# Kernel optimization log

Measured on AMD Instinct MI355X. Metric: run time of the kernel, lower is better.

The kernel has to match this reference:

```python
import jax, jax.numpy as jnp
import numpy as np

B, S, D, F = 8, 2048, 256, 8

def setup_inputs() -> dict:
    key = jax.random.key(0)
    ks = jax.random.split(key, 7)
    hidden_states = jax.random.normal(ks[0], (B, S, D), dtype=jnp.float32)
    # flat indices into zero-prepended [1 + B*S, D] token table; 0 = padding row
    select_idx = jax.random.randint(ks[1], (B, S, F), 0, B * S + 1, dtype=jnp.int32)
    word_mask = jax.random.randint(ks[2], (B, S), 0, 2, dtype=jnp.int32)
    W1 = jax.random.normal(ks[3], (D, D), dtype=jnp.float32) * (1.0 / np.sqrt(D))
    b1 = jax.random.normal(ks[4], (D,), dtype=jnp.float32) * 0.02
    w2 = jax.random.normal(ks[5], (D,), dtype=jnp.float32) * (1.0 / np.sqrt(D))
    b2 = jax.random.normal(ks[6], (1,), dtype=jnp.float32) * 0.02
    return {"hidden_states": hidden_states, "select_idx": select_idx,
            "word_mask": word_mask, "W1": W1, "b1": b1, "w2": w2, "b2": b2}

def reference(hidden_states, select_idx, word_mask, W1, b1, w2, b2):
    b, s, d = hidden_states.shape
    h = jnp.tanh(hidden_states.reshape(-1, d) @ W1.T + b1)          # [B*S, D]
    h = jnp.concatenate([jnp.zeros((1, d), h.dtype), h], axis=0)    # zero padding row at index 0
    g = h[select_idx.reshape(-1)]                                    # gather: [B*S*F, D]
    g = g.reshape(b * s, -1, d).max(axis=1)                          # AdaptiveMaxPool1d(1) over word occurrences
    scores = (g @ w2 + b2[0]).reshape(b, s)                          # w2 linear -> [B, S]
    neg = -10000.0 * (1.0 - word_mask.astype(jnp.float32))
    return scores.astype(jnp.float32) + neg
```

## Files before the change

kernel.cpp:

```cpp
#include <hip/hip_runtime.h>
#include <hip/hip_bf16.h>
#include <math.h>

#define BB 8
#define SS 2048
#define DD 256
#define FF 8
#define NTOK (BB*SS)

typedef __bf16 bf16x8 __attribute__((ext_vector_type(8)));
typedef float  f32x4  __attribute__((ext_vector_type(4)));
typedef float  f32x2  __attribute__((ext_vector_type(2)));

#define BM 128
#define BN 64
#define BK 64
#define NSTEP (DD/BK)
#define XS 72

__device__ __forceinline__ float fast_tanh(float x) {
    float e = __expf(2.0f * x);
    return 1.0f - 2.0f * __builtin_amdgcn_rcpf(e + 1.0f);
}

__device__ __forceinline__ unsigned pack2_bf16(float a, float b) {
    return (__float_as_uint(a) >> 16) | (__float_as_uint(b) & 0xFFFF0000u);
}

__device__ __forceinline__ unsigned char f32_to_fp8(float v) {
    return (unsigned char)(__builtin_amdgcn_cvt_pk_fp8_f32(v, v, 0, false) & 0xFF);
}

__global__ __launch_bounds__(512, 4) void gemm_tanh_kernel(
    const float* __restrict__ x, const float* __restrict__ W1,
    const float* __restrict__ b1, unsigned char* __restrict__ table)
{
    __shared__ __align__(16) unsigned short xs[2][BM * XS];
    __shared__ __align__(16) unsigned short wsb[2][BN * XS];

    const int tid  = threadIdx.x;
    const int bx   = blockIdx.x;
    const int tokgrp = bx & 127;
    const int nblk   = bx >> 7;
    const int tok0 = tokgrp * BM;
    const int n0   = nblk * BN;

    if (bx == 0 && tid < 64) ((unsigned int*)table)[tid] = 0u;

    const int wave = tid >> 6, lane = tid & 63;
    const int wm = wave >> 1;
    const int wn = wave & 1;
    const int lr = lane & 15;
    const int kg = lane >> 4;

    f32x4 xr[4], wr[2];

    auto load_chunk = [&](int k0) {
        #pragma unroll
        for (int rep = 0; rep < 4; ++rep) {
            int slot = rep * 512 + tid;
            int row = slot >> 4, kc = slot & 15;
            xr[rep] = *(const f32x4*)&x[(size_t)(tok0 + row) * DD + k0 + kc * 4];
        }
        #pragma unroll
        for (int rep = 0; rep < 2; ++rep) {
            int slot = rep * 512 + tid;
            int row = slot >> 4, kc = slot & 15;
            wr[rep] = *(const f32x4*)&W1[(size_t)(n0 + row) * DD + k0 + kc * 4];
        }
    };
    auto store_lds = [&](int buf) {
        #pragma unroll
        for (int rep = 0; rep < 4; ++rep) {
            int slot = rep * 512 + tid;
            int row = slot >> 4, kc = slot & 15;
            uint2 p;
            p.x = pack2_bf16(xr[rep].x, xr[rep].y);
            p.y = pack2_bf16(xr[rep].z, xr[rep].w);
            *(uint2*)&xs[buf][row * XS + kc * 4] = p;
        }
        #pragma unroll
        for (int rep = 0; rep < 2; ++rep) {
            int slot = rep * 512 + tid;
            int row = slot >> 4, kc = slot & 15;
            uint2 p;
            p.x = pack2_bf16(wr[rep].x, wr[rep].y);
            p.y = pack2_bf16(wr[rep].z, wr[rep].w);
            *(uint2*)&wsb[buf][row * XS + kc * 4] = p;
        }
    };

    f32x4 acc[2][2];
    #pragma unroll
    for (int mf = 0; mf < 2; ++mf)
        #pragma unroll
        for (int nf = 0; nf < 2; ++nf)
            acc[mf][nf] = (f32x4){0.f, 0.f, 0.f, 0.f};

    load_chunk(0);
    store_lds(0);

    for (int s = 0; s < NSTEP; ++s) {
        __syncthreads();
        const int buf = s & 1;
        if (s + 1 < NSTEP) load_chunk((s + 1) * BK);

        bf16x8 af[2][2], bfr[2][2];
        #pragma unroll
        for (int c = 0; c < 2; ++c) {
            #pragma unroll
            for (int mf = 0; mf < 2; ++mf) {
                int m = wm * 32 + mf * 16 + lr;
                af[c][mf] = *(const bf16x8*)&xs[buf][m * XS + c * 32 + kg * 8];
            }
            #pragma unroll
            for (int nf = 0; nf < 2; ++nf) {
                int n = wn * 32 + nf * 16 + lr;
                bfr[c][nf] = *(const bf16x8*)&wsb[buf][n * XS + c * 32 + kg * 8];
            }
        }
        if (s + 1 < NSTEP) store_lds(buf ^ 1);

        #pragma unroll
        for (int c = 0; c < 2; ++c)
            #pragma unroll
            for (int mf = 0; mf < 2; ++mf)
                #pragma unroll
                for (int nf = 0; nf < 2; ++nf)
                    acc[mf][nf] = __builtin_amdgcn_mfma_f32_16x16x32_bf16(
                        af[c][mf], bfr[c][nf], acc[mf][nf], 0, 0, 0);
    }

    float bj[2];
    #pragma unroll
    for (int nf = 0; nf < 2; ++nf) bj[nf] = b1[n0 + wn * 32 + nf * 16 + lr];

    __syncthreads();
    unsigned char* sc = (unsigned char*)&xs[0][0];
    #pragma unroll
    for (int mf = 0; mf < 2; ++mf) {
        #pragma unroll
        for (int r = 0; r < 4; ++r) {
            int m = wm * 32 + mf * 16 + kg * 4 + r;
            #pragma unroll
            for (int nf = 0; nf < 2; ++nf) {
                float v = fast_tanh(acc[mf][nf][r] + bj[nf]);
                sc[m * 80 + wn * 32 + nf * 16 + lr] = f32_to_fp8(v);
            }
        }
    }
    __syncthreads();
    {
        int row = tid >> 2;
        int off = (tid & 3) * 16;
        uint4 v = *(const uint4*)&sc[row * 80 + off];
        *(uint4*)&table[(size_t)(1 + tok0 + row) * DD + n0 + off] = v;
    }
}

__global__ __launch_bounds__(256) void gather_score_kernel(
    const unsigned char* __restrict__ table,
    const int* __restrict__ select_idx,
    const int* __restrict__ word_mask,
    const float* __restrict__ w2,
    const float* __restrict__ b2,
    float* __restrict__ out)
{
    const int tid  = threadIdx.x;
    const int lane = tid & 63;
    const int wv   = tid >> 6;
    const int i    = blockIdx.x * 4 + wv;
    const int half = lane >> 5;
    const int c    = lane & 31;
    const int d0   = c * 8;

    const int4* sp = (const int4*)(select_idx + (size_t)i * FF);
    int4 q0 = sp[0], q1 = sp[1];
    int rows[4];
    rows[0] = half ? q0.y : q0.x;
    rows[1] = half ? q0.w : q0.z;
    rows[2] = half ? q1.y : q1.x;
    rows[3] = half ? q1.w : q1.z;

    float m[8];
    #pragma unroll
    for (int j = 0; j < 8; ++j) m[j] = -INFINITY;

    #pragma unroll
    for (int it = 0; it < 4; ++it) {
        uint2 u = *(const uint2*)(table + (size_t)rows[it] * DD + d0);
        f32x2 a0 = __builtin_amdgcn_cvt_pk_f32_fp8(u.x, false);
        f32x2 a1 = __builtin_amdgcn_cvt_pk_f32_fp8(u.x, true);
        f32x2 a2 = __builtin_amdgcn_cvt_pk_f32_fp8(u.y, false);
        f32x2 a3 = __builtin_amdgcn_cvt_pk_f32_fp8(u.y, true);
        m[0] = fmaxf(m[0], a0.x); m[1] = fmaxf(m[1], a0.y);
        m[2] = fmaxf(m[2], a1.x); m[3] = fmaxf(m[3], a1.y);
        m[4] = fmaxf(m[4], a2.x); m[5] = fmaxf(m[5], a2.y);
        m[6] = fmaxf(m[6], a3.x); m[7] = fmaxf(m[7], a3.y);
    }

    #pragma unroll
    for (int j = 0; j < 8; ++j) m[j] = fmaxf(m[j], __shfl_xor(m[j], 32));

    f32x4 wa = *(const f32x4*)&w2[d0];
    f32x4 wb = *(const f32x4*)&w2[d0 + 4];
    float p = m[0] * wa.x + m[1] * wa.y + m[2] * wa.z + m[3] * wa.w
            + m[4] * wb.x + m[5] * wb.y + m[6] * wb.z + m[7] * wb.w;

    #pragma unroll
    for (int off = 16; off; off >>= 1) p += __shfl_xor(p, off);

    if (lane == 0) {
        float neg = word_mask[i] ? 0.f : -10000.f;
        out[i] = p + b2[0] + neg;
    }
}

extern "C" void kernel_launch(void* const* d_in, const int* in_sizes, int n_in,
                              void* d_out, int out_size, void* d_ws, size_t ws_size,
                              hipStream_t stream) {
    const float* hs    = (const float*)d_in[0];
    const int*   sidx  = (const int*)  d_in[1];
    const int*   wmask = (const int*)  d_in[2];
    const float* W1    = (const float*)d_in[3];
    const float* b1    = (const float*)d_in[4];
    const float* w2    = (const float*)d_in[5];
    const float* b2    = (const float*)d_in[6];
    float* out = (float*)d_out;

    unsigned char* table = (unsigned char*)d_ws;

    gemm_tanh_kernel<<<(NTOK / BM) * (DD / BN), 512, 0, stream>>>(hs, W1, b1, table);
    gather_score_kernel<<<NTOK / 4, 256, 0, stream>>>(table, sidx, wmask, w2, b2, out);
}
```

Baseline: 87.63 us.

## Hold token rows in registers and stream all W1 columns through swizzled LDS

Restructures the GEMM so each block owns 64 tokens across all 256 output features. The x rows are loaded once into registers as bf16 MFMA fragments, instead of being re-read by four separate n-blocks. W1 is streamed in 64-row chunks through a double-buffered, XOR-swizzled LDS tile. This cuts global traffic on hidden_states, but every block now rereads all of W1 and the grid shrinks to 256 large blocks, which may underuse the GPU.

```diff
diff --git a/kernel.cpp b/kernel.cpp
--- a/kernel.cpp
+++ b/kernel.cpp
@@ -12,11 +12,9 @@
 typedef float  f32x4  __attribute__((ext_vector_type(4)));
 typedef float  f32x2  __attribute__((ext_vector_type(2)));
 
-#define BM 128
-#define BN 64
-#define BK 64
-#define NSTEP (DD/BK)
-#define XS 72
+#define BM 64
+#define CH 64
+#define NCH (DD/CH)
 
 __device__ __forceinline__ float fast_tanh(float x) {
     float e = __expf(2.0f * x);
@@ -31,19 +29,15 @@
     return (unsigned char)(__builtin_amdgcn_cvt_pk_fp8_f32(v, v, 0, false) & 0xFF);
 }
 
-__global__ __launch_bounds__(512, 4) void gemm_tanh_kernel(
+__global__ __launch_bounds__(512, 2) void gemm_tanh_kernel(
     const float* __restrict__ x, const float* __restrict__ W1,
     const float* __restrict__ b1, unsigned char* __restrict__ table)
 {
-    __shared__ __align__(16) unsigned short xs[2][BM * XS];
-    __shared__ __align__(16) unsigned short wsb[2][BN * XS];
+    __shared__ __align__(16) unsigned short wt[2][CH * DD];
 
     const int tid  = threadIdx.x;
     const int bx   = blockIdx.x;
-    const int tokgrp = bx & 127;
-    const int nblk   = bx >> 7;
-    const int tok0 = tokgrp * BM;
-    const int n0   = nblk * BN;
+    const int tok0 = bx * BM;
 
     if (bx == 0 && tid < 64) ((unsigned int*)table)[tid] = 0u;
 
@@ -53,108 +47,114 @@
     const int lr = lane & 15;
     const int kg = lane >> 4;
 
-    f32x4 xr[4], wr[2];
-
-    auto load_chunk = [&](int k0) {
-        #pragma unroll
-        for (int rep = 0; rep < 4; ++rep) {
-            int slot = rep * 512 + tid;
-            int row = slot >> 4, kc = slot & 15;
-            xr[rep] = *(const f32x4*)&x[(size_t)(tok0 + row) * DD + k0 + kc * 4];
-        }
-        #pragma unroll
-        for (int rep = 0; rep < 2; ++rep) {
-            int slot = rep * 512 + tid;
-            int row = slot >> 4, kc = slot & 15;
-            wr[rep] = *(const f32x4*)&W1[(size_t)(n0 + row) * DD + k0 + kc * 4];
-        }
+    const float* xrow = x + (size_t)(tok0 + wm * 16 + lr) * DD + kg * 8;
+    f32x4 xa[8], xb[8];
+    #pragma unroll
+    for (int c = 0; c < 8; ++c) {
+        xa[c] = *(const f32x4*)&xrow[c * 32];
+        xb[c] = *(const f32x4*)&xrow[c * 32 + 4];
+    }
+
+    const int srow = tid >> 3;
+    const int scol = (tid & 7) * 32;
+    f32x4 wr0[8], wrn[8];
+
+    auto wload = [&](int nc, f32x4* wr) {
+        const float* wsrc = W1 + (size_t)(nc * CH + srow) * DD + scol;
+        #pragma unroll
+        for (int j = 0; j < 8; ++j) wr[j] = *(const f32x4*)&wsrc[j * 4];
     };
-    auto store_lds = [&](int buf) {
-        #pragma unroll
-        for (int rep = 0; rep < 4; ++rep) {
-            int slot = rep * 512 + tid;
-            int row = slot >> 4, kc = slot & 15;
-            uint2 p;
-            p.x = pack2_bf16(xr[rep].x, xr[rep].y);
-            p.y = pack2_bf16(xr[rep].z, xr[rep].w);
-            *(uint2*)&xs[buf][row * XS + kc * 4] = p;
-        }
-        #pragma unroll
-        for (int rep = 0; rep < 2; ++rep) {
-            int slot = rep * 512 + tid;
-            int row = slot >> 4, kc = slot & 15;
-            uint2 p;
-            p.x = pack2_bf16(wr[rep].x, wr[rep].y);
-            p.y = pack2_bf16(wr[rep].z, wr[rep].w);
-            *(uint2*)&wsb[buf][row * XS + kc * 4] = p;
+    auto wstore = [&](int buf, const f32x4* wr) {
+        #pragma unroll
+        for (int j = 0; j < 4; ++j) {
+            uint4 p;
+            p.x = pack2_bf16(wr[2*j].x,   wr[2*j].y);
+            p.y = pack2_bf16(wr[2*j].z,   wr[2*j].w);
+            p.z = pack2_bf16(wr[2*j+1].x, wr[2*j+1].y);
+            p.w = pack2_bf16(wr[2*j+1].z, wr[2*j+1].w);
+            int q  = (scol >> 3) + j;
+            int qp = q ^ (srow & 7);
+            *(uint4*)&wt[buf][srow * DD + qp * 8] = p;
         }
     };
 
-    f32x4 acc[2][2];
-    #pragma unroll
-    for (int mf = 0; mf < 2; ++mf)
+    wload(0, wr0);
+
+    bf16x8 af[8];
+    #pragma unroll
+    for (int c = 0; c < 8; ++c) {
+        uint4 p;
+        p.x = pack2_bf16(xa[c].x, xa[c].y);
+        p.y = pack2_bf16(xa[c].z, xa[c].w);
+        p.z = pack2_bf16(xb[c].x, xb[c].y);
+        p.w = pack2_bf16(xb[c].z, xb[c].w);
+        af[c] = *(bf16x8*)&p;
+    }
+
+    wstore(0, wr0);
+    __syncthreads();
+
+    f32x4 acc[NCH][2];
+    #pragma unroll
+    for (int nc = 0; nc < NCH; ++nc)
         #pragma unroll
         for (int nf = 0; nf < 2; ++nf)
-            acc[mf][nf] = (f32x4){0.f, 0.f, 0.f, 0.f};
-
-    load_chunk(0);
-    store_lds(0);
-
-    for (int s = 0; s < NSTEP; ++s) {
-        __syncthreads();
-        const int buf = s & 1;
-        if (s + 1 < NSTEP) load_chunk((s + 1) * BK);
-
-        bf16x8 af[2][2], bfr[2][2];
-        #pragma unroll
-        for (int c = 0; c < 2; ++c) {
+            acc[nc][nf] = (f32x4){0.f, 0.f, 0.f, 0.f};
+
+    const int nl0 = wn * 32 + lr;
+    const int nl1 = nl0 + 16;
+    const int sw  = lr & 7;
+
+    #pragma unroll
+    for (int nc = 0; nc < NCH; ++nc) {
+        const int buf = nc & 1;
+        if (nc + 1 < NCH) wload(nc + 1, wrn);
+
+        #pragma unroll
+        for (int c = 0; c < 8; ++c) {
+            int q  = c * 4 + kg;
+            int qp = q ^ sw;
+            bf16x8 bf0 = *(const bf16x8*)&wt[buf][nl0 * DD + qp * 8];
+            bf16x8 bf1 = *(const bf16x8*)&wt[buf][nl1 * DD + qp * 8];
+            acc[nc][0] = __builtin_amdgcn_mfma_f32_16x16x32_bf16(af[c], bf0, acc[nc][0], 0, 0, 0);
+            acc[nc][1] = __builtin_amdgcn_mfma_f32_16x16x32_bf16(af[c], bf1, acc[nc][1], 0, 0, 0);
+        }
+
+        if (nc + 1 < NCH) {
+            wstore(buf ^ 1, wrn);
+            __syncthreads();
+        }
+    }
+
+    float bj[NCH][2];
+    #pragma unroll
+    for (int nc = 0; nc < NCH; ++nc) {
+        bj[nc][0] = b1[nc * CH + wn * 32 + lr];
+        bj[nc][1] = b1[nc * CH + wn * 32 + 16 + lr];
+    }
+
+    unsigned char* sc = (unsigned char*)&wt[0][0];
+    #pragma unroll
+    for (int nc = 0; nc < NCH; ++nc) {
+        #pragma unroll
+        for (int nf = 0; nf < 2; ++nf) {
             #pragma unroll
-            for (int mf = 0; mf < 2; ++mf) {
-                int m = wm * 32 + mf * 16 + lr;
-                af[c][mf] = *(const bf16x8*)&xs[buf][m * XS + c * 32 + kg * 8];
-            }
-            #pragma unroll
-            for (int nf = 0; nf < 2; ++nf) {
-                int n = wn * 32 + nf * 16 + lr;
-                bfr[c][nf] = *(const bf16x8*)&wsb[buf][n * XS + c * 32 + kg * 8];
-            }
-        }
-        if (s + 1 < NSTEP) store_lds(buf ^ 1);
-
-        #pragma unroll
-        for (int c = 0; c < 2; ++c)
-            #pragma unroll
-            for (int mf = 0; mf < 2; ++mf)
-                #pragma unroll
-                for (int nf = 0; nf < 2; ++nf)
-                    acc[mf][nf] = __builtin_amdgcn_mfma_f32_16x16x32_bf16(
-                        af[c][mf], bfr[c][nf], acc[mf][nf], 0, 0, 0);
-    }
-
-    float bj[2];
-    #pragma unroll
-    for (int nf = 0; nf < 2; ++nf) bj[nf] = b1[n0 + wn * 32 + nf * 16 + lr];
-
-    __syncthreads();
-    unsigned char* sc = (unsigned char*)&xs[0][0];
-    #pragma unroll
-    for (int mf = 0; mf < 2; ++mf) {
-        #pragma unroll
-        for (int r = 0; r < 4; ++r) {
-            int m = wm * 32 + mf * 16 + kg * 4 + r;
-            #pragma unroll
-            for (int nf = 0; nf < 2; ++nf) {
-                float v = fast_tanh(acc[mf][nf][r] + bj[nf]);
-                sc[m * 80 + wn * 32 + nf * 16 + lr] = f32_to_fp8(v);
+            for (int r = 0; r < 4; ++r) {
+                int row = wm * 16 + kg * 4 + r;
+                int col = nc * CH + wn * 32 + nf * 16 + lr;
+                float v = fast_tanh(acc[nc][nf][r] + bj[nc][nf]);
+                sc[row * 272 + col] = f32_to_fp8(v);
             }
         }
     }
     __syncthreads();
     {
-        int row = tid >> 2;
-        int off = (tid & 3) * 16;
-        uint4 v = *(const uint4*)&sc[row * 80 + off];
-        *(uint4*)&table[(size_t)(1 + tok0 + row) * DD + n0 + off] = v;
+        int row = tid >> 3;
+        int off = (tid & 7) * 32;
+        uint4 v0 = *(const uint4*)&sc[row * 272 + off];
+        uint4 v1 = *(const uint4*)&sc[row * 272 + off + 16];
+        *(uint4*)&table[(size_t)(1 + tok0 + row) * DD + off]      = v0;
+        *(uint4*)&table[(size_t)(1 + tok0 + row) * DD + off + 16] = v1;
     }
 }
 
@@ -230,6 +230,6 @@
 
     unsigned char* table = (unsigned char*)d_ws;
 
-    gemm_tanh_kernel<<<(NTOK / BM) * (DD / BN), 512, 0, stream>>>(hs, W1, b1, table);
+    gemm_tanh_kernel<<<NTOK / BM, 512, 0, stream>>>(hs, W1, b1, table);
     gather_score_kernel<<<NTOK / 4, 256, 0, stream>>>(table, sidx, wmask, w2, b2, out);
 }
```

New measurement: 96.88 us. 10.6% more time.
